# Optimization experiments

Hardware: AMD Instinct MI355X
Metric: run time of the kernel (lower is better)

Reference implementation:

```python
import jax, jax.numpy as jnp
import numpy as np

B, L, D, H, NB = 64, 30, 512, 8, 6
AS, MT = 18, 4096
T = 3 * L
HD = D // H
EPS = 1e-3  # keras LayerNormalization default epsilon
CONV_FEAT = 7 * 7 * 64  # 84 ->(8,s4) 20 ->(4,s2) 9 ->(3,s1) 7


def setup_inputs() -> dict:
    key = jax.random.key(0)
    ks = iter(jax.random.split(key, 64))
    r = lambda *s: jax.random.normal(next(ks), s, jnp.float32) * 0.02
    inp = {
        'rtgs': jax.random.normal(next(ks), (B, L, 1), jnp.float32),
        'states': jax.random.uniform(next(ks), (B, L, 84, 84, 4), jnp.float32) * 255.0,
        'actions': jax.random.randint(next(ks), (B, L, 1), 0, AS),
        'timesteps': jax.random.randint(next(ks), (B, 1, 1), 0, MT + 1),
        # rtg embedding
        'W_rtg': r(1, D), 'b_rtg': r(D),
        # state conv stem (HWIO)
        'conv1_w': r(8, 8, 4, 32), 'conv1_b': r(32),
        'conv2_w': r(4, 4, 32, 64), 'conv2_b': r(64),
        'conv3_w': r(3, 3, 64, 64), 'conv3_b': r(64),
        'dense_s_w': r(CONV_FEAT, D), 'dense_s_b': r(D),
        # action embedding table
        'emb_a': r(AS, D),
        # positional embeddings
        'abs_pos': r(1, MT + 1, D), 'rel_pos': r(1, T + 1, D),
        # decoder blocks (stacked over NB)
        'ln1_g': 1.0 + r(NB, D), 'ln1_b': r(NB, D),
        'Wk': r(NB, D, D), 'bk': r(NB, D),
        'Wq': r(NB, D, D), 'bq': r(NB, D),
        'Wv': r(NB, D, D), 'bv': r(NB, D),
        'ln2_g': 1.0 + r(NB, D), 'ln2_b': r(NB, D),
        'W1': r(NB, D, 4 * D), 'b1': r(NB, 4 * D),
        'W2': r(NB, 4 * D, D), 'b2': r(NB, D),
        # final norm + head (no bias)
        'lnf_g': 1.0 + r(D), 'lnf_b': r(D),
        'W_head': r(D, AS),
    }
    return inp


def _conv(x, w, b, stride):
    y = jax.lax.conv_general_dilated(x, w, (stride, stride), 'VALID',
                                     dimension_numbers=('NHWC', 'HWIO', 'NHWC'))
    return jax.nn.relu(y + b)


def _layernorm(x, g, b):
    m = x.mean(-1, keepdims=True)
    v = ((x - m) ** 2).mean(-1, keepdims=True)
    return (x - m) / jnp.sqrt(v + EPS) * g + b


def _attn(x, Wk, bk, Wq, bq, Wv, bv):
    Bx, Tx, C = x.shape
    split = lambda z: z.reshape(Bx, Tx, H, HD).transpose(0, 2, 1, 3)  # (B,H,T,hd)
    k, q, v = split(x @ Wk + bk), split(x @ Wq + bq), split(x @ Wv + bv)
    # NOTE: faithful to source: scores = K @ Q^T (not Q @ K^T)
    s = jnp.einsum('bhid,bhjd->bhij', k, q) / jnp.sqrt(jnp.float32(HD))
    mask = jnp.tril(jnp.ones((Tx, Tx), bool))
    s = jnp.where(mask, s, -jnp.inf)
    w = jax.nn.softmax(s, axis=-1)
    o = jnp.einsum('bhij,bhjd->bhid', w, v)
    return o.transpose(0, 2, 1, 3).reshape(Bx, Tx, C)


def reference(rtgs, states, actions, timesteps, W_rtg, b_rtg,
              conv1_w, conv1_b, conv2_w, conv2_b, conv3_w, conv3_b,
              dense_s_w, dense_s_b, emb_a, abs_pos, rel_pos,
              ln1_g, ln1_b, Wk, bk, Wq, bq, Wv, bv,
              ln2_g, ln2_b, W1, b1, W2, b2, lnf_g, lnf_b, W_head):
    # embeddings
    rtg_e = jnp.tanh(rtgs @ W_rtg + b_rtg)                       # (B,L,D)
    s = states.reshape(B * L, 84, 84, 4) / 255.0
    s = _conv(s, conv1_w, conv1_b, 4)
    s = _conv(s, conv2_w, conv2_b, 2)
    s = _conv(s, conv3_w, conv3_b, 1)
    st_e = jnp.tanh(s.reshape(B, L, -1) @ dense_s_w + dense_s_b)  # (B,L,D)
    a_e = jnp.tanh(emb_a[actions[..., 0]])                        # (B,L,D)
    # positional: abs gathered at start timestep + relative
    abs_e = abs_pos[0][timesteps[:, 0, 0]][:, None, :]            # (B,1,D)
    pos = rel_pos[:, :T, :] + abs_e                               # (B,3L,D)
    # interleave (rtg, state, action) per timestep
    tokens = jnp.stack([rtg_e, st_e, a_e], axis=2).reshape(B, T, D)
    x = tokens + pos
    for i in range(NB):
        h = _layernorm(x, ln1_g[i], ln1_b[i])
        x = x + _attn(h, Wk[i], bk[i], Wq[i], bq[i], Wv[i], bv[i])
        h = _layernorm(x, ln2_g[i], ln2_b[i])
        x = x + jax.nn.gelu(h @ W1[i] + b1[i], approximate=False) @ W2[i] + b2[i]
    x = _layernorm(x, lnf_g, lnf_b)
    logits = x @ W_head                                           # (B,3L,AS)
    return logits[:, 1::3, :]                                     # state positions -> (B,L,AS)
```

## Files before the change

kernel.cpp:

```cpp
#include <hip/hip_runtime.h>
#include <hip/hip_bf16.h>

typedef __attribute__((ext_vector_type(8))) __bf16 bf16x8;
typedef __attribute__((ext_vector_type(4))) float f32x4;

#define ACT_NONE 0
#define ACT_RELU 1
#define ACT_GELU 2
#define ACT_TANH 3
#define OUT_F32 0
#define OUT_BF16 1
#define OUT_ADD 2

__device__ __forceinline__ void gll16(const void* g, void* l) {
  __builtin_amdgcn_global_load_lds(
      reinterpret_cast<const __attribute__((address_space(1))) unsigned int*>(
          reinterpret_cast<unsigned long long>(g)),
      reinterpret_cast<__attribute__((address_space(3))) unsigned int*>(
          reinterpret_cast<unsigned long long>(l)),
      16, 0, 0);
}

__device__ __forceinline__ int xcd_swz(int bid, int n) {
  const int q = n >> 3, r = n & 7, x = bid & 7, o = bid >> 3;
  return (x < r ? x * (q + 1) : r * (q + 1) + (x - r) * q) + o;
}

template<int MODE, int K>
__device__ __forceinline__ size_t a_rowbase(int m) {
  if constexpr (MODE == 0) {
    return (size_t)m * K;
  } else if constexpr (MODE == 1) {
    int img = m / 400; int p = m - img * 400; int oy = p / 20; int ox = p - oy * 20;
    return (size_t)img * 28224 + oy * 1344 + ox * 16;
  } else if constexpr (MODE == 2) {
    int img = m / 81; int p = m - img * 81; int oy = p / 9; int ox = p - oy * 9;
    return (size_t)img * 12800 + oy * 1280 + ox * 64;
  } else {
    int img = m / 49; int p = m - img * 49; int oy = p / 7; int ox = p - oy * 7;
    return (size_t)img * 5184 + oy * 576 + ox * 64;
  }
}
template<int MODE>
__device__ __forceinline__ int f_koff(int kb) {
  if constexpr (MODE == 0) return kb;
  else if constexpr (MODE == 2) return (kb >> 7) * 640 + ((kb >> 5) & 3) * 32;
  else return kb + (kb / 192) * 384;
}

__device__ __forceinline__ bf16x8 ld8f(const float* f) {
  float4 a = *(const float4*)f;
  float4 b = *(const float4*)(f + 4);
  bf16x8 r;
  r[0] = (__bf16)a.x; r[1] = (__bf16)a.y; r[2] = (__bf16)a.z; r[3] = (__bf16)a.w;
  r[4] = (__bf16)b.x; r[5] = (__bf16)b.y; r[6] = (__bf16)b.z; r[7] = (__bf16)b.w;
  return r;
}

__device__ __forceinline__ float act_apply(float v, int ACT) {
  if (ACT == ACT_RELU) return fmaxf(v, 0.f);
  if (ACT == ACT_GELU) return 0.5f * v * (1.f + erff(v * 0.70710678118f));
  if (ACT == ACT_TANH) return tanhf(v);
  return v;
}

template<int MODE, int TM, int TN, int WM, int WN, int K, int ACT, int OUTM, int LDC, int NBLK, int SWZ>
__global__ __launch_bounds__(256) void gemm_k(const __bf16* __restrict__ A,
                                              const __bf16* __restrict__ BT,
                                              const float* __restrict__ bias,
                                              void* __restrict__ C) {
  constexpr int SM = TM / WM, SN = TN / WN;
  constexpr int AM = SM / 16, AN = SN / 16;
  constexpr int TA = TM / 64, TB = TN / 64;
  __shared__ __align__(16) __bf16 As[TM * 32];
  __shared__ __align__(16) __bf16 Bs[TN * 32];
  const int tid = threadIdx.x;
  const int wave = tid >> 6, lane = tid & 63;
  const int quad = lane >> 4, l16 = lane & 15;
  const int wr = wave % WM, wc = wave / WM;
  const int bid = SWZ ? xcd_swz(blockIdx.x, gridDim.x) : blockIdx.x;
  const int bn = bid % NBLK, bm = bid / NBLK;
  const int m0 = bm * TM, n0 = bn * TN;
  const int lrow = lane >> 2, lkc = lane & 3;

  const __bf16* ga[TA];
  const __bf16* gb[TB];
#pragma unroll
  for (int t = 0; t < TA; ++t)
    ga[t] = A + a_rowbase<MODE, K>(m0 + (wave + 4 * t) * 16 + lrow) + lkc * 8;
#pragma unroll
  for (int t = 0; t < TB; ++t)
    gb[t] = BT + (size_t)(n0 + (wave + 4 * t) * 16 + lrow) * K + lkc * 8;

  f32x4 acc[AM][AN] = {};
  for (int kt = 0; kt < K / 32; ++kt) {
    const int kb = kt * 32;
    const int fa = f_koff<MODE>(kb);
    __syncthreads();
#pragma unroll
    for (int t = 0; t < TA; ++t)
      gll16(ga[t] + fa, &As[(wave + 4 * t) * 16 * 32]);
#pragma unroll
    for (int t = 0; t < TB; ++t)
      gll16(gb[t] + kb, &Bs[(wave + 4 * t) * 16 * 32]);
    __syncthreads();
    bf16x8 af[AM], bf[AN];
#pragma unroll
    for (int mt = 0; mt < AM; ++mt)
      af[mt] = *(const bf16x8*)&As[(wr * SM + mt * 16 + l16) * 32 + quad * 8];
#pragma unroll
    for (int nt = 0; nt < AN; ++nt)
      bf[nt] = *(const bf16x8*)&Bs[(wc * SN + nt * 16 + l16) * 32 + quad * 8];
#pragma unroll
    for (int mt = 0; mt < AM; ++mt)
#pragma unroll
      for (int nt = 0; nt < AN; ++nt)
        acc[mt][nt] = __builtin_amdgcn_mfma_f32_16x16x32_bf16(af[mt], bf[nt], acc[mt][nt], 0, 0, 0);
  }

#pragma unroll
  for (int nt = 0; nt < AN; ++nt) {
    const int col = n0 + wc * SN + nt * 16 + l16;
    const float bvl = bias[col];
#pragma unroll
    for (int mt = 0; mt < AM; ++mt) {
#pragma unroll
      for (int r = 0; r < 4; ++r) {
        const int row = m0 + wr * SM + mt * 16 + quad * 4 + r;
        float v = act_apply(acc[mt][nt][r] + bvl, ACT);
        const size_t off = (size_t)row * LDC + col;
        if constexpr (OUTM == OUT_F32) ((float*)C)[off] = v;
        else if constexpr (OUTM == OUT_BF16) ((__bf16*)C)[off] = (__bf16)v;
        else ((float*)C)[off] += v;
      }
    }
  }
}

__global__ __launch_bounds__(256) void conv1_k(const float* __restrict__ A,
                                               const __bf16* __restrict__ BT,
                                               const float* __restrict__ bias,
                                               __bf16* __restrict__ C) {
  __shared__ __align__(16) __bf16 As[128 * 32];
  __shared__ __align__(16) __bf16 Bs[32 * 32];
  const int tid = threadIdx.x;
  const int wave = tid >> 6, lane = tid & 63;
  const int quad = lane >> 4, l16 = lane & 15;
  const int m0 = xcd_swz(blockIdx.x, gridDim.x) * 128;
  const int lrow = lane >> 2, lkc = lane & 3;
  const int r0 = tid >> 2, k0o = (tid & 3) * 8;
  const int r1 = r0 + 64;
  const size_t ar0 = a_rowbase<1, 256>(m0 + r0);
  const size_t ar1 = a_rowbase<1, 256>(m0 + r1);
  const __bf16* gB = BT + (size_t)(wave * 16 + lrow) * 256 + lkc * 8;

  f32x4 acc[2][2] = {};
  bf16x8 a0 = ld8f(A + ar0 + k0o);
  bf16x8 a1 = ld8f(A + ar1 + k0o);
  for (int kt = 0; kt < 8; ++kt) {
    const int kb = kt * 32;
    __syncthreads();
    if (wave < 2) gll16(gB + kb, &Bs[wave * 16 * 32]);
    *(bf16x8*)&As[r0 * 32 + k0o] = a0;
    *(bf16x8*)&As[r1 * 32 + k0o] = a1;
    __syncthreads();
    if (kt < 7) {
      const int fa = (kt + 1) * 336;
      a0 = ld8f(A + ar0 + fa + k0o);
      a1 = ld8f(A + ar1 + fa + k0o);
    }
    bf16x8 af[2], bf[2];
#pragma unroll
    for (int mt = 0; mt < 2; ++mt)
      af[mt] = *(const bf16x8*)&As[(wave * 32 + mt * 16 + l16) * 32 + quad * 8];
#pragma unroll
    for (int nt = 0; nt < 2; ++nt)
      bf[nt] = *(const bf16x8*)&Bs[(nt * 16 + l16) * 32 + quad * 8];
#pragma unroll
    for (int mt = 0; mt < 2; ++mt)
#pragma unroll
      for (int nt = 0; nt < 2; ++nt)
        acc[mt][nt] = __builtin_amdgcn_mfma_f32_16x16x32_bf16(af[mt], bf[nt], acc[mt][nt], 0, 0, 0);
  }
#pragma unroll
  for (int nt = 0; nt < 2; ++nt) {
    const int col = nt * 16 + l16;
    const float bvl = bias[col];
#pragma unroll
    for (int mt = 0; mt < 2; ++mt) {
#pragma unroll
      for (int r = 0; r < 4; ++r) {
        const int row = m0 + wave * 32 + mt * 16 + quad * 4 + r;
        C[(size_t)row * 32 + col] = (__bf16)fmaxf(acc[mt][nt][r] + bvl, 0.f);
      }
    }
  }
}

template<typename TO>
__global__ void transpose_pad(const float* __restrict__ src, TO* __restrict__ dst,
                              int R, int C, int Cpad, long long sz, long long dz, float scale) {
  src += blockIdx.z * sz; dst += blockIdx.z * dz;
  __shared__ float t[32][33];
  const int tx = threadIdx.x, ty = threadIdx.y;
  const int r0 = blockIdx.x * 32, c0 = blockIdx.y * 32;
  for (int i = ty; i < 32; i += 8) {
    int r = r0 + i, c = c0 + tx;
    t[i][tx] = (r < R && c < C) ? src[(size_t)r * C + c] : 0.f;
  }
  __syncthreads();
  for (int i = ty; i < 32; i += 8) {
    int c = c0 + i, r = r0 + tx;
    if (c < Cpad && r < R)
      dst[(size_t)c * R + r] = (c < C) ? (TO)(t[tx][i] * scale) : (TO)0.f;
  }
}

__global__ void transpose_qkv(const float* __restrict__ Wk_, const float* __restrict__ Wq_,
                              const float* __restrict__ Wv_, __bf16* __restrict__ dst) {
  const int z = blockIdx.z, which = z / 6, i = z - which * 6;
  const float* src = (which == 0 ? Wk_ : which == 1 ? Wq_ : Wv_) + (size_t)i * 512 * 512;
  __bf16* d = dst + (size_t)i * 1536 * 512;
  __shared__ float t[32][33];
  const int tx = threadIdx.x, ty = threadIdx.y;
  const int r0 = blockIdx.x * 32, c0 = blockIdx.y * 32;
  for (int j = ty; j < 32; j += 8)
    t[j][tx] = src[(size_t)(r0 + j) * 512 + c0 + tx];
  __syncthreads();
  for (int j = ty; j < 32; j += 8) {
    const int c = c0 + j;
    const int row = ((c >> 6) * 192) + which * 64 + (c & 63);
    d[(size_t)row * 512 + r0 + tx] = (__bf16)t[tx][j];
  }
}

__global__ void biascat_k(const float* bk, const float* bq, const float* bv, float* dst) {
  const int i = blockIdx.x;
  for (int d = threadIdx.x; d < 512; d += 256) {
    const int g = (d >> 6) * 192 + (d & 63);
    dst[i * 1536 + g] = bk[i * 512 + d];
    dst[i * 1536 + g + 64] = bq[i * 512 + d];
    dst[i * 1536 + g + 128] = bv[i * 512 + d];
  }
}

__global__ void embed_k(const float* __restrict__ rtgs, const int* __restrict__ actions,
                        const int* __restrict__ timesteps, const float* __restrict__ W_rtg,
                        const float* __restrict__ b_rtg, const float* __restrict__ emb_a,
                        const float* __restrict__ abs_pos, const float* __restrict__ rel_pos,
                        const float* __restrict__ ste, float* __restrict__ x) {
  const int idx = blockIdx.x * 256 + threadIdx.x;
  const int d = idx & 511; const int rb = idx >> 9;
  const int b = rb / 96, t = rb - b * 96;
  if (t >= 90) { x[idx] = 0.f; return; }
  const int l = t / 3, r = t - l * 3;
  const float pos = rel_pos[t * 512 + d] + abs_pos[(size_t)timesteps[b] * 512 + d];
  float tok;
  if (r == 0) tok = tanhf(rtgs[b * 30 + l] * W_rtg[d] + b_rtg[d]);
  else if (r == 1) tok = ste[(size_t)(b * 30 + l) * 512 + d];
  else tok = tanhf(emb_a[actions[b * 30 + l] * 512 + d]);
  x[idx] = tok + pos;
}

__global__ __launch_bounds__(256) void ln_k(const float* __restrict__ x, const float* __restrict__ g,
                                            const float* __restrict__ bb, __bf16* __restrict__ h) {
  const int row = blockIdx.x * 4 + (threadIdx.x >> 6);
  const int lane = threadIdx.x & 63;
  const float* xr = x + (size_t)row * 512;
  float4 a = *(const float4*)&xr[lane * 8];
  float4 c = *(const float4*)&xr[lane * 8 + 4];
  float vv[8] = {a.x, a.y, a.z, a.w, c.x, c.y, c.z, c.w};
  float s = 0.f, q = 0.f;
#pragma unroll
  for (int j = 0; j < 8; ++j) { s += vv[j]; q += vv[j] * vv[j]; }
  for (int o = 32; o; o >>= 1) { s += __shfl_xor(s, o); q += __shfl_xor(q, o); }
  const float mean = s * (1.f / 512.f);
  const float var = q * (1.f / 512.f) - mean * mean;
  const float rstd = rsqrtf(var + 1e-3f);
  float4 g1 = *(const float4*)&g[lane * 8];
  float4 g2 = *(const float4*)&g[lane * 8 + 4];
  float4 b1 = *(const float4*)&bb[lane * 8];
  float4 b2 = *(const float4*)&bb[lane * 8 + 4];
  float gg[8] = {g1.x, g1.y, g1.z, g1.w, g2.x, g2.y, g2.z, g2.w};
  float bbv[8] = {b1.x, b1.y, b1.z, b1.w, b2.x, b2.y, b2.z, b2.w};
  bf16x8 ov;
#pragma unroll
  for (int j = 0; j < 8; ++j)
    ov[j] = (__bf16)((vv[j] - mean) * rstd * gg[j] + bbv[j]);
  *(bf16x8*)&h[(size_t)row * 512 + lane * 8] = ov;
}

__global__ __launch_bounds__(256) void qkvattn_k(const __bf16* __restrict__ A,
                                                 const __bf16* __restrict__ BTh,
                                                 const float* __restrict__ bias,
                                                 float* __restrict__ x) {
  __shared__ __align__(16) char smem[64512];
  __bf16* kS = (__bf16*)smem;
  __bf16* qS = (__bf16*)(smem + 13824);
  __bf16* wS = (__bf16*)smem;
  float* sS = (float*)(smem + 27648);
  __bf16* vT = (__bf16*)(smem + 27648);
  __bf16* As = (__bf16*)(smem + 27648);
  __bf16* Bs = (__bf16*)(smem + 27648 + 6144);

  const int tid = threadIdx.x;
  const int b = blockIdx.x >> 3, h = blockIdx.x & 7;
  const int wave = tid >> 6, lane = tid & 63, quad = lane >> 4, l16 = lane & 15;
  const int wr = wave & 1, wc = wave >> 1;
  const int lrow = lane >> 2, lkc = lane & 3;

  const __bf16* ga0 = A + (size_t)(b * 96 + wave * 16 + lrow) * 512 + lkc * 8;
  const __bf16* ga1 = A + (size_t)(b * 96 + ((wave & 1) + 4) * 16 + lrow) * 512 + lkc * 8;
  const __bf16* gbp[3];
#pragma unroll
  for (int t = 0; t < 3; ++t)
    gbp[t] = BTh + (size_t)(h * 192 + (wave + 4 * t) * 16 + lrow) * 512 + lkc * 8;

  f32x4 acc[3][6] = {};
  for (int kt = 0; kt < 16; ++kt) {
    const int kb = kt * 32;
    __syncthreads();
    gll16(ga0 + kb, &As[wave * 16 * 32]);
    if (wave < 2) gll16(ga1 + kb, &As[(wave + 4) * 16 * 32]);
#pragma unroll
    for (int t = 0; t < 3; ++t)
      gll16(gbp[t] + kb, &Bs[(wave + 4 * t) * 16 * 32]);
    __syncthreads();
    bf16x8 af[3], bq[6];
#pragma unroll
    for (int mt = 0; mt < 3; ++mt)
      af[mt] = *(const bf16x8*)&As[(wr * 48 + mt * 16 + l16) * 32 + quad * 8];
#pragma unroll
    for (int nt = 0; nt < 6; ++nt)
      bq[nt] = *(const bf16x8*)&Bs[(wc * 96 + nt * 16 + l16) * 32 + quad * 8];
#pragma unroll
    for (int mt = 0; mt < 3; ++mt)
#pragma unroll
      for (int nt = 0; nt < 6; ++nt)
        acc[mt][nt] = __builtin_amdgcn_mfma_f32_16x16x32_bf16(af[mt], bq[nt], acc[mt][nt], 0, 0, 0);
  }

#pragma unroll
  for (int nt = 0; nt < 6; ++nt) {
    const int col = wc * 96 + nt * 16 + l16;
    if (col < 128) {
      const float bvl = bias[h * 192 + col];
#pragma unroll
      for (int mt = 0; mt < 3; ++mt) {
#pragma unroll
        for (int r = 0; r < 4; ++r) {
          const int row = wr * 48 + mt * 16 + quad * 4 + r;
          const float v = acc[mt][nt][r] + bvl;
          if (col < 64) kS[row * 72 + col] = (__bf16)v;
          else qS[row * 72 + (col - 64)] = (__bf16)v;
        }
      }
    }
  }
  __syncthreads();

  for (int tt = wave; tt < 36; tt += 4) {
    const int it = tt / 6, jt = tt - it * 6;
    f32x4 sacc = {0.f, 0.f, 0.f, 0.f};
#pragma unroll
    for (int ks = 0; ks < 2; ++ks) {
      bf16x8 af = *(const bf16x8*)&kS[(it * 16 + l16) * 72 + ks * 32 + quad * 8];
      bf16x8 bq = *(const bf16x8*)&qS[(jt * 16 + l16) * 72 + ks * 32 + quad * 8];
      sacc = __builtin_amdgcn_mfma_f32_16x16x32_bf16(af, bq, sacc, 0, 0, 0);
    }
    const int col = jt * 16 + l16;
#pragma unroll
    for (int r = 0; r < 4; ++r) {
      const int row = it * 16 + quad * 4 + r;
      sS[row * 96 + col] = (col <= row && col < 90) ? sacc[r] * 0.125f : -1e30f;
    }
  }
  __syncthreads();

  for (int row = wave; row < 96; row += 4) {
    const float e0 = sS[row * 96 + lane];
    const float e1 = (lane < 32) ? sS[row * 96 + 64 + lane] : -1e30f;
    float m = fmaxf(e0, e1);
    for (int o = 32; o; o >>= 1) m = fmaxf(m, __shfl_xor(m, o));
    const float p0 = __expf(e0 - m);
    const float p1 = (lane < 32) ? __expf(e1 - m) : 0.f;
    float s = p0 + p1;
    for (int o = 32; o; o >>= 1) s += __shfl_xor(s, o);
    const float inv = 1.f / s;
    wS[row * 104 + lane] = (__bf16)(p0 * inv);
    if (lane < 32) wS[row * 104 + 64 + lane] = (__bf16)(p1 * inv);
  }
  __syncthreads();

  if (wc == 1) {
#pragma unroll
    for (int nt = 2; nt < 6; ++nt) {
      const int vd = nt * 16 + l16 - 32;
      const float bvl = bias[h * 192 + 128 + vd];
#pragma unroll
      for (int mt = 0; mt < 3; ++mt) {
#pragma unroll
        for (int r = 0; r < 4; ++r) {
          const int row = wr * 48 + mt * 16 + quad * 4 + r;
          vT[vd * 104 + row] = (__bf16)(acc[mt][nt][r] + bvl);
        }
      }
    }
  }
  __syncthreads();

  for (int tt = wave; tt < 24; tt += 4) {
    const int it = tt >> 2, dt = tt & 3;
    f32x4 pacc = {0.f, 0.f, 0.f, 0.f};
#pragma unroll
    for (int ks = 0; ks < 3; ++ks) {
      bf16x8 aw = *(const bf16x8*)&wS[(it * 16 + l16) * 104 + ks * 32 + quad * 8];
      bf16x8 bv = *(const bf16x8*)&vT[(dt * 16 + l16) * 104 + ks * 32 + quad * 8];
      pacc = __builtin_amdgcn_mfma_f32_16x16x32_bf16(aw, bv, pacc, 0, 0, 0);
    }
    const int d = dt * 16 + l16;
#pragma unroll
    for (int r = 0; r < 4; ++r) {
      const int i = it * 16 + quad * 4 + r;
      if (i < 90) {
        float* p = x + (size_t)(b * 96 + i) * 512 + h * 64 + d;
        *p += pacc[r];
      }
    }
  }
}

__global__ __launch_bounds__(64) void head_k(const float* __restrict__ x, const float* __restrict__ g,
                                             const float* __restrict__ bb, const float* __restrict__ whT,
                                             float* __restrict__ out) {
  const int m = blockIdx.x;
  const int b = m / 30, l = m - b * 30;
  const float* xr = x + (size_t)(b * 96 + 3 * l + 1) * 512;
  const int lane = threadIdx.x;
  float4 a = *(const float4*)&xr[lane * 8];
  float4 c = *(const float4*)&xr[lane * 8 + 4];
  float vv[8] = {a.x, a.y, a.z, a.w, c.x, c.y, c.z, c.w};
  float s = 0.f, q = 0.f;
#pragma unroll
  for (int j = 0; j < 8; ++j) { s += vv[j]; q += vv[j] * vv[j]; }
  for (int o = 32; o; o >>= 1) { s += __shfl_xor(s, o); q += __shfl_xor(q, o); }
  const float mean = s * (1.f / 512.f);
  const float var = q * (1.f / 512.f) - mean * mean;
  const float rstd = rsqrtf(var + 1e-3f);
  float4 g1 = *(const float4*)&g[lane * 8];
  float4 g2 = *(const float4*)&g[lane * 8 + 4];
  float4 b1 = *(const float4*)&bb[lane * 8];
  float4 b2 = *(const float4*)&bb[lane * 8 + 4];
  float gg[8] = {g1.x, g1.y, g1.z, g1.w, g2.x, g2.y, g2.z, g2.w};
  float bbv[8] = {b1.x, b1.y, b1.z, b1.w, b2.x, b2.y, b2.z, b2.w};
#pragma unroll
  for (int j = 0; j < 8; ++j)
    vv[j] = (vv[j] - mean) * rstd * gg[j] + bbv[j];
  for (int aa = 0; aa < 18; ++aa) {
    float4 w1v = *(const float4*)&whT[aa * 512 + lane * 8];
    float4 w2v = *(const float4*)&whT[aa * 512 + lane * 8 + 4];
    float ww[8] = {w1v.x, w1v.y, w1v.z, w1v.w, w2v.x, w2v.y, w2v.z, w2v.w};
    float d = 0.f;
#pragma unroll
    for (int j = 0; j < 8; ++j) d += vv[j] * ww[j];
    for (int o = 32; o; o >>= 1) d += __shfl_xor(d, o);
    if (lane == 0) out[m * 18 + aa] = d;
  }
}

extern "C" void kernel_launch(void* const* d_in, const int* in_sizes, int n_in,
                              void* d_out, int out_size, void* d_ws, size_t ws_size,
                              hipStream_t stream) {
  const float* rtgs = (const float*)d_in[0];
  const float* states = (const float*)d_in[1];
  const int* actions = (const int*)d_in[2];
  const int* timesteps = (const int*)d_in[3];
  const float* W_rtg = (const float*)d_in[4];
  const float* b_rtg = (const float*)d_in[5];
  const float* conv1_w = (const float*)d_in[6];
  const float* conv1_b = (const float*)d_in[7];
  const float* conv2_w = (const float*)d_in[8];
  const float* conv2_b = (const float*)d_in[9];
  const float* conv3_w = (const float*)d_in[10];
  const float* conv3_b = (const float*)d_in[11];
  const float* dense_s_w = (const float*)d_in[12];
  const float* dense_s_b = (const float*)d_in[13];
  const float* emb_a = (const float*)d_in[14];
  const float* abs_pos = (const float*)d_in[15];
  const float* rel_pos = (const float*)d_in[16];
  const float* ln1_g = (const float*)d_in[17];
  const float* ln1_b = (const float*)d_in[18];
  const float* Wk = (const float*)d_in[19];
  const float* bk = (const float*)d_in[20];
  const float* Wq = (const float*)d_in[21];
  const float* bq = (const float*)d_in[22];
  const float* Wv = (const float*)d_in[23];
  const float* bv = (const float*)d_in[24];
  const float* ln2_g = (const float*)d_in[25];
  const float* ln2_b = (const float*)d_in[26];
  const float* W1 = (const float*)d_in[27];
  const float* b1 = (const float*)d_in[28];
  const float* W2 = (const float*)d_in[29];
  const float* b2 = (const float*)d_in[30];
  const float* lnf_g = (const float*)d_in[31];
  const float* lnf_b = (const float*)d_in[32];
  const float* W_head = (const float*)d_in[33];
  float* out = (float*)d_out;

  char* W = (char*)d_ws;
  float* x = (float*)(W + 0);
  __bf16* h = (__bf16*)(W + 12582912);
  __bf16* qkvT = (__bf16*)(W + 18874368);
  __bf16* w1T = (__bf16*)(W + 28311552);
  __bf16* w2T = (__bf16*)(W + 40894464);
  __bf16* dswT = (__bf16*)(W + 53477376);
  __bf16* c1wT = (__bf16*)(W + 56688640);
  __bf16* c2wT = (__bf16*)(W + 56754176);
  __bf16* c3wT = (__bf16*)(W + 56885248);
  float* whT = (float*)(W + 57032704);
  float* bqkv = (float*)(W + 57069568);
  __bf16* c1out = (__bf16*)(W + 57106432);
  __bf16* c2out = (__bf16*)(W + 106258432);
  __bf16* c3out = (__bf16*)(W + 57106432);
  float* ste = (float*)(W + 69148672);
  __bf16* mlph = (__bf16*)(W + 57106432);

  const dim3 tb(32, 8);
  transpose_pad<__bf16><<<dim3(8, 4, 1), tb, 0, stream>>>(conv1_w, c1wT, 256, 32, 128, 0, 0, 1.f / 255.f);
  transpose_pad<__bf16><<<dim3(16, 4, 1), tb, 0, stream>>>(conv2_w, c2wT, 512, 64, 128, 0, 0, 1.f);
  transpose_pad<__bf16><<<dim3(18, 4, 1), tb, 0, stream>>>(conv3_w, c3wT, 576, 64, 128, 0, 0, 1.f);
  transpose_pad<__bf16><<<dim3(98, 16, 1), tb, 0, stream>>>(dense_s_w, dswT, 3136, 512, 512, 0, 0, 1.f);
  transpose_qkv<<<dim3(16, 16, 18), tb, 0, stream>>>(Wk, Wq, Wv, qkvT);
  transpose_pad<__bf16><<<dim3(16, 64, 6), tb, 0, stream>>>(W1, w1T, 512, 2048, 2048, 512 * 2048, 2048 * 512, 1.f);
  transpose_pad<__bf16><<<dim3(64, 16, 6), tb, 0, stream>>>(W2, w2T, 2048, 512, 512, 2048 * 512, 512 * 2048, 1.f);
  transpose_pad<float><<<dim3(16, 1, 1), tb, 0, stream>>>(W_head, whT, 512, 18, 18, 0, 0, 1.f);
  biascat_k<<<6, 256, 0, stream>>>(bk, bq, bv, bqkv);

  conv1_k<<<6000, 256, 0, stream>>>(states, c1wT, conv1_b, c1out);
  gemm_k<2, 128, 64, 2, 2, 512, ACT_RELU, OUT_BF16, 64, 1, 1><<<1215, 256, 0, stream>>>(c1out, c2wT, conv2_b, c2out);
  gemm_k<3, 128, 64, 2, 2, 576, ACT_RELU, OUT_BF16, 64, 1, 1><<<735, 256, 0, stream>>>(c2out, c3wT, conv3_b, c3out);
  gemm_k<0, 64, 64, 2, 2, 3136, ACT_TANH, OUT_F32, 512, 8, 1><<<240, 256, 0, stream>>>(c3out, dswT, dense_s_b, (void*)ste);

  embed_k<<<12288, 256, 0, stream>>>(rtgs, actions, timesteps, W_rtg, b_rtg, emb_a, abs_pos, rel_pos, ste, x);

  for (int i = 0; i < 6; ++i) {
    ln_k<<<1536, 256, 0, stream>>>(x, ln1_g + i * 512, ln1_b + i * 512, h);
    qkvattn_k<<<512, 256, 0, stream>>>(h, qkvT + (size_t)i * 1536 * 512, bqkv + i * 1536, x);
    ln_k<<<1536, 256, 0, stream>>>(x, ln2_g + i * 512, ln2_b + i * 512, h);
    gemm_k<0, 128, 128, 2, 2, 512, ACT_GELU, OUT_BF16, 2048, 16, 1><<<768, 256, 0, stream>>>(
        h, w1T + (size_t)i * 2048 * 512, b1 + i * 2048, mlph);
    gemm_k<0, 64, 64, 2, 2, 2048, ACT_NONE, OUT_ADD, 512, 8, 1><<<768, 256, 0, stream>>>(
        mlph, w2T + (size_t)i * 2048 * 512, b2 + i * 512, x);
  }

  head_k<<<1920, 64, 0, stream>>>(x, lnf_g, lnf_b, whT, out);
}
```

Measured before the change: 1.294 ms.

## Fuse LN1 into QKV-attention kernel and merge weight prep into one launch

Removes the separate ln_k launch before attention. Each attention block now computes the per-row mean and rstd of its batch's 96 rows itself, then normalizes fp32 x on the fly into the bf16 A tile in LDS, prefetching the next k-slice into registers. All weight transposes and the bias concatenation are merged into a single prep kernel dispatched by block index, cutting about nine launches to one. The block index is also XCD-swizzled. The cost is that each of the 8 head blocks per batch redundantly reads and reduces the same rows, and the fused A-tile path does more ALU work inside the k-loop.

```diff
diff --git a/kernel.cpp b/kernel.cpp
--- a/kernel.cpp
+++ b/kernel.cpp
@@ -197,13 +197,12 @@
   }
 }
 
-template<typename TO>
-__global__ void transpose_pad(const float* __restrict__ src, TO* __restrict__ dst,
-                              int R, int C, int Cpad, long long sz, long long dz, float scale) {
-  src += blockIdx.z * sz; dst += blockIdx.z * dz;
+__device__ __forceinline__ void tp32(const float* __restrict__ src, int R, int C, int Cpad,
+                                     int bx, int by, float scale, int mode, int which,
+                                     __bf16* dB, float* dF) {
   __shared__ float t[32][33];
-  const int tx = threadIdx.x, ty = threadIdx.y;
-  const int r0 = blockIdx.x * 32, c0 = blockIdx.y * 32;
+  const int tx = threadIdx.x & 31, ty = threadIdx.x >> 5;
+  const int r0 = bx * 32, c0 = by * 32;
   for (int i = ty; i < 32; i += 8) {
     int r = r0 + i, c = c0 + tx;
     t[i][tx] = (r < R && c < C) ? src[(size_t)r * C + c] : 0.f;
@@ -211,36 +210,66 @@
   __syncthreads();
   for (int i = ty; i < 32; i += 8) {
     int c = c0 + i, r = r0 + tx;
-    if (c < Cpad && r < R)
-      dst[(size_t)c * R + r] = (c < C) ? (TO)(t[tx][i] * scale) : (TO)0.f;
-  }
-}
-
-__global__ void transpose_qkv(const float* __restrict__ Wk_, const float* __restrict__ Wq_,
-                              const float* __restrict__ Wv_, __bf16* __restrict__ dst) {
-  const int z = blockIdx.z, which = z / 6, i = z - which * 6;
-  const float* src = (which == 0 ? Wk_ : which == 1 ? Wq_ : Wv_) + (size_t)i * 512 * 512;
-  __bf16* d = dst + (size_t)i * 1536 * 512;
-  __shared__ float t[32][33];
-  const int tx = threadIdx.x, ty = threadIdx.y;
-  const int r0 = blockIdx.x * 32, c0 = blockIdx.y * 32;
-  for (int j = ty; j < 32; j += 8)
-    t[j][tx] = src[(size_t)(r0 + j) * 512 + c0 + tx];
-  __syncthreads();
-  for (int j = ty; j < 32; j += 8) {
-    const int c = c0 + j;
-    const int row = ((c >> 6) * 192) + which * 64 + (c & 63);
-    d[(size_t)row * 512 + r0 + tx] = (__bf16)t[tx][j];
-  }
-}
-
-__global__ void biascat_k(const float* bk, const float* bq, const float* bv, float* dst) {
-  const int i = blockIdx.x;
+    if (c < Cpad && r < R) {
+      float v = (c < C) ? t[tx][i] * scale : 0.f;
+      if (mode == 2) {
+        const int row = ((c >> 6) * 192) + which * 64 + (c & 63);
+        dB[(size_t)row * 512 + r] = (__bf16)v;
+      } else if (mode == 1) {
+        dF[(size_t)c * R + r] = v;
+      } else {
+        dB[(size_t)c * R + r] = (__bf16)v;
+      }
+    }
+  }
+}
+
+__global__ __launch_bounds__(256) void prep_k(
+    const float* c1w, const float* c2w, const float* c3w, const float* dsw,
+    const float* Wk_, const float* Wq_, const float* Wv_,
+    const float* W1_, const float* W2_, const float* Wh_,
+    const float* bk_, const float* bq_, const float* bv_,
+    __bf16* c1wT, __bf16* c2wT, __bf16* c3wT, __bf16* dswT, __bf16* qkvT,
+    __bf16* w1T, __bf16* w2T, float* whT, float* bqkv) {
+  int bid = blockIdx.x;
+  if (bid < 32) { tp32(c1w, 256, 32, 128, bid & 7, bid >> 3, 1.f / 255.f, 0, 0, c1wT, nullptr); return; }
+  bid -= 32;
+  if (bid < 64) { tp32(c2w, 512, 64, 128, bid & 15, bid >> 4, 1.f, 0, 0, c2wT, nullptr); return; }
+  bid -= 64;
+  if (bid < 72) { tp32(c3w, 576, 64, 128, bid % 18, bid / 18, 1.f, 0, 0, c3wT, nullptr); return; }
+  bid -= 72;
+  if (bid < 1568) { tp32(dsw, 3136, 512, 512, bid % 98, bid / 98, 1.f, 0, 0, dswT, nullptr); return; }
+  bid -= 1568;
+  if (bid < 4608) {
+    const int bx = bid & 15, by = (bid >> 4) & 15, z = bid >> 8;
+    const int which = z / 6, i = z - which * 6;
+    const float* s = (which == 0 ? Wk_ : which == 1 ? Wq_ : Wv_) + (size_t)i * 512 * 512;
+    tp32(s, 512, 512, 512, bx, by, 1.f, 2, which, qkvT + (size_t)i * 1536 * 512, nullptr);
+    return;
+  }
+  bid -= 4608;
+  if (bid < 6144) {
+    const int bx = bid & 15, by = (bid >> 4) & 63, z = bid >> 10;
+    tp32(W1_ + (size_t)z * 512 * 2048, 512, 2048, 2048, bx, by, 1.f, 0, 0,
+         w1T + (size_t)z * 2048 * 512, nullptr);
+    return;
+  }
+  bid -= 6144;
+  if (bid < 6144) {
+    const int bx = bid & 63, by = (bid >> 6) & 15, z = bid >> 10;
+    tp32(W2_ + (size_t)z * 2048 * 512, 2048, 512, 512, bx, by, 1.f, 0, 0,
+         w2T + (size_t)z * 512 * 2048, nullptr);
+    return;
+  }
+  bid -= 6144;
+  if (bid < 16) { tp32(Wh_, 512, 18, 18, bid, 0, 1.f, 1, 0, nullptr, whT); return; }
+  bid -= 16;
+  const int i = bid;
   for (int d = threadIdx.x; d < 512; d += 256) {
     const int g = (d >> 6) * 192 + (d & 63);
-    dst[i * 1536 + g] = bk[i * 512 + d];
-    dst[i * 1536 + g + 64] = bq[i * 512 + d];
-    dst[i * 1536 + g + 128] = bv[i * 512 + d];
+    bqkv[i * 1536 + g] = bk_[i * 512 + d];
+    bqkv[i * 1536 + g + 64] = bq_[i * 512 + d];
+    bqkv[i * 1536 + g + 128] = bv_[i * 512 + d];
   }
 }
 
@@ -290,10 +319,27 @@
   *(bf16x8*)&h[(size_t)row * 512 + lane * 8] = ov;
 }
 
-__global__ __launch_bounds__(256) void qkvattn_k(const __bf16* __restrict__ A,
-                                                 const __bf16* __restrict__ BTh,
-                                                 const float* __restrict__ bias,
-                                                 float* __restrict__ x) {
+__device__ __forceinline__ bf16x8 lnpack8(float4 a, float4 c, float mean, float rstd,
+                                          const float* gS, const float* bS, int c0) {
+  float4 g1 = *(const float4*)&gS[c0], g2 = *(const float4*)&gS[c0 + 4];
+  float4 b1 = *(const float4*)&bS[c0], b2 = *(const float4*)&bS[c0 + 4];
+  bf16x8 o;
+  o[0] = (__bf16)((a.x - mean) * rstd * g1.x + b1.x);
+  o[1] = (__bf16)((a.y - mean) * rstd * g1.y + b1.y);
+  o[2] = (__bf16)((a.z - mean) * rstd * g1.z + b1.z);
+  o[3] = (__bf16)((a.w - mean) * rstd * g1.w + b1.w);
+  o[4] = (__bf16)((c.x - mean) * rstd * g2.x + b2.x);
+  o[5] = (__bf16)((c.y - mean) * rstd * g2.y + b2.y);
+  o[6] = (__bf16)((c.z - mean) * rstd * g2.z + b2.z);
+  o[7] = (__bf16)((c.w - mean) * rstd * g2.w + b2.w);
+  return o;
+}
+
+__global__ __launch_bounds__(256) void lnqkvattn_k(float* x,
+                                                   const float* __restrict__ g,
+                                                   const float* __restrict__ bb,
+                                                   const __bf16* __restrict__ BTh,
+                                                   const float* __restrict__ bias) {
   __shared__ __align__(16) char smem[64512];
   __bf16* kS = (__bf16*)smem;
   __bf16* qS = (__bf16*)(smem + 13824);
@@ -301,31 +347,78 @@
   float* sS = (float*)(smem + 27648);
   __bf16* vT = (__bf16*)(smem + 27648);
   __bf16* As = (__bf16*)(smem + 27648);
-  __bf16* Bs = (__bf16*)(smem + 27648 + 6144);
+  __bf16* Bs = (__bf16*)(smem + 33792);
+  float* mS = (float*)(smem + 46080);
+  float* rS = (float*)(smem + 46464);
+  float* gS = (float*)(smem + 46848);
+  float* bS = (float*)(smem + 48896);
 
   const int tid = threadIdx.x;
-  const int b = blockIdx.x >> 3, h = blockIdx.x & 7;
+  const int bidw = xcd_swz(blockIdx.x, gridDim.x);
+  const int b = bidw >> 3, h = bidw & 7;
   const int wave = tid >> 6, lane = tid & 63, quad = lane >> 4, l16 = lane & 15;
   const int wr = wave & 1, wc = wave >> 1;
   const int lrow = lane >> 2, lkc = lane & 3;
-
-  const __bf16* ga0 = A + (size_t)(b * 96 + wave * 16 + lrow) * 512 + lkc * 8;
-  const __bf16* ga1 = A + (size_t)(b * 96 + ((wave & 1) + 4) * 16 + lrow) * 512 + lkc * 8;
+  const float* xb = x + (size_t)(b * 96) * 512;
+
+  for (int d = tid; d < 512; d += 256) { gS[d] = g[d]; bS[d] = bb[d]; }
+  for (int rr = wave * 4 + quad; rr < 96; rr += 16) {
+    const float* xr = xb + (size_t)rr * 512 + l16 * 32;
+    float s = 0.f, q = 0.f;
+#pragma unroll
+    for (int j = 0; j < 8; ++j) {
+      float4 v = *(const float4*)&xr[j * 4];
+      s += v.x + v.y + v.z + v.w;
+      q += v.x * v.x + v.y * v.y + v.z * v.z + v.w * v.w;
+    }
+#pragma unroll
+    for (int o = 8; o; o >>= 1) { s += __shfl_xor(s, o, 16); q += __shfl_xor(q, o, 16); }
+    if (l16 == 0) {
+      const float mean = s * (1.f / 512.f);
+      const float var = q * (1.f / 512.f) - mean * mean;
+      mS[rr] = mean;
+      rS[rr] = rsqrtf(var + 1e-3f);
+    }
+  }
+  __syncthreads();
+
   const __bf16* gbp[3];
 #pragma unroll
   for (int t = 0; t < 3; ++t)
     gbp[t] = BTh + (size_t)(h * 192 + (wave + 4 * t) * 16 + lrow) * 512 + lkc * 8;
+
+  const int ur = tid >> 2, uc = (tid & 3) * 8;
+  const float mv0 = mS[ur], rv0 = rS[ur];
+  float mv1 = 0.f, rv1 = 0.f;
+  if (tid < 128) { mv1 = mS[ur + 64]; rv1 = rS[ur + 64]; }
+  float4 p0a = *(const float4*)&xb[(size_t)ur * 512 + uc];
+  float4 p0b = *(const float4*)&xb[(size_t)ur * 512 + uc + 4];
+  float4 p1a = {0.f, 0.f, 0.f, 0.f}, p1b = {0.f, 0.f, 0.f, 0.f};
+  if (tid < 128) {
+    p1a = *(const float4*)&xb[(size_t)(ur + 64) * 512 + uc];
+    p1b = *(const float4*)&xb[(size_t)(ur + 64) * 512 + uc + 4];
+  }
 
   f32x4 acc[3][6] = {};
   for (int kt = 0; kt < 16; ++kt) {
     const int kb = kt * 32;
     __syncthreads();
-    gll16(ga0 + kb, &As[wave * 16 * 32]);
-    if (wave < 2) gll16(ga1 + kb, &As[(wave + 4) * 16 * 32]);
 #pragma unroll
     for (int t = 0; t < 3; ++t)
       gll16(gbp[t] + kb, &Bs[(wave + 4 * t) * 16 * 32]);
+    *(bf16x8*)&As[ur * 32 + uc] = lnpack8(p0a, p0b, mv0, rv0, gS, bS, kb + uc);
+    if (tid < 128)
+      *(bf16x8*)&As[(ur + 64) * 32 + uc] = lnpack8(p1a, p1b, mv1, rv1, gS, bS, kb + uc);
     __syncthreads();
+    if (kt < 15) {
+      const int nb = kb + 32 + uc;
+      p0a = *(const float4*)&xb[(size_t)ur * 512 + nb];
+      p0b = *(const float4*)&xb[(size_t)ur * 512 + nb + 4];
+      if (tid < 128) {
+        p1a = *(const float4*)&xb[(size_t)(ur + 64) * 512 + nb];
+        p1b = *(const float4*)&xb[(size_t)(ur + 64) * 512 + nb + 4];
+      }
+    }
     bf16x8 af[3], bq[6];
 #pragma unroll
     for (int mt = 0; mt < 3; ++mt)
@@ -525,16 +618,9 @@
   float* ste = (float*)(W + 69148672);
   __bf16* mlph = (__bf16*)(W + 57106432);
 
-  const dim3 tb(32, 8);
-  transpose_pad<__bf16><<<dim3(8, 4, 1), tb, 0, stream>>>(conv1_w, c1wT, 256, 32, 128, 0, 0, 1.f / 255.f);
-  transpose_pad<__bf16><<<dim3(16, 4, 1), tb, 0, stream>>>(conv2_w, c2wT, 512, 64, 128, 0, 0, 1.f);
-  transpose_pad<__bf16><<<dim3(18, 4, 1), tb, 0, stream>>>(conv3_w, c3wT, 576, 64, 128, 0, 0, 1.f);
-  transpose_pad<__bf16><<<dim3(98, 16, 1), tb, 0, stream>>>(dense_s_w, dswT, 3136, 512, 512, 0, 0, 1.f);
-  transpose_qkv<<<dim3(16, 16, 18), tb, 0, stream>>>(Wk, Wq, Wv, qkvT);
-  transpose_pad<__bf16><<<dim3(16, 64, 6), tb, 0, stream>>>(W1, w1T, 512, 2048, 2048, 512 * 2048, 2048 * 512, 1.f);
-  transpose_pad<__bf16><<<dim3(64, 16, 6), tb, 0, stream>>>(W2, w2T, 2048, 512, 512, 2048 * 512, 512 * 2048, 1.f);
-  transpose_pad<float><<<dim3(16, 1, 1), tb, 0, stream>>>(W_head, whT, 512, 18, 18, 0, 0, 1.f);
-  biascat_k<<<6, 256, 0, stream>>>(bk, bq, bv, bqkv);
+  prep_k<<<18654, 256, 0, stream>>>(conv1_w, conv2_w, conv3_w, dense_s_w, Wk, Wq, Wv,
+                                    W1, W2, W_head, bk, bq, bv,
+                                    c1wT, c2wT, c3wT, dswT, qkvT, w1T, w2T, whT, bqkv);
 
   conv1_k<<<6000, 256, 0, stream>>>(states, c1wT, conv1_b, c1out);
   gemm_k<2, 128, 64, 2, 2, 512, ACT_RELU, OUT_BF16, 64, 1, 1><<<1215, 256, 0, stream>>>(c1out, c2wT, conv2_b, c2out);
@@ -544,8 +630,8 @@
   embed_k<<<12288, 256, 0, stream>>>(rtgs, actions, timesteps, W_rtg, b_rtg, emb_a, abs_pos, rel_pos, ste, x);
 
   for (int i = 0; i < 6; ++i) {
-    ln_k<<<1536, 256, 0, stream>>>(x, ln1_g + i * 512, ln1_b + i * 512, h);
-    qkvattn_k<<<512, 256, 0, stream>>>(h, qkvT + (size_t)i * 1536 * 512, bqkv + i * 1536, x);
+    lnqkvattn_k<<<512, 256, 0, stream>>>(x, ln1_g + i * 512, ln1_b + i * 512,
+                                         qkvT + (size_t)i * 1536 * 512, bqkv + i * 1536);
     ln_k<<<1536, 256, 0, stream>>>(x, ln2_g + i * 512, ln2_b + i * 512, h);
     gemm_k<0, 128, 128, 2, 2, 512, ACT_GELU, OUT_BF16, 2048, 16, 1><<<768, 256, 0, stream>>>(
         h, w1T + (size_t)i * 2048 * 512, b1 + i * 2048, mlph);
```

Measured after the change: 1.292 ms. Within noise of the previous version (-0.2%).
